# Optimization experiments

Measured on AMD Instinct MI355X. Metric: run time of the kernel, lower is better.

## Reference

```python
import jax, jax.numpy as jnp
from jax import lax
import numpy as np

EPS = 1e-5  # BatchNorm eps; eval-mode BN with running_mean=0, running_var=1


def _conv(x, w, b):
    return lax.conv_general_dilated(x, w, (1, 1), 'SAME', dimension_numbers=('NCHW', 'OIHW', 'NCHW')) + b[None, :, None, None]


def _cbr(x, w, b, g, a):
    # Conv -> BN(eval, mean=0, var=1) -> ReLU
    y = _conv(x, w, b)
    y = g[None, :, None, None] * (y * (1.0 / np.sqrt(1.0 + EPS))) + a[None, :, None, None]
    return jax.nn.relu(y)


def _pool(x):
    return lax.reduce_window(x, -jnp.inf, lax.max, (1, 1, 2, 2), (1, 1, 2, 2), 'VALID')


def _up2(x):
    B, C, H, W = x.shape
    Ho, Wo = 2 * H, 2 * W
    ys = jnp.arange(Ho) * ((H - 1) / (Ho - 1))
    xs = jnp.arange(Wo) * ((W - 1) / (Wo - 1))
    y0 = jnp.floor(ys).astype(jnp.int32); y1 = jnp.minimum(y0 + 1, H - 1)
    x0 = jnp.floor(xs).astype(jnp.int32); x1 = jnp.minimum(x0 + 1, W - 1)
    wy = (ys - y0).astype(x.dtype); wx = (xs - x0).astype(x.dtype)
    row = x[:, :, y0, :] * (1 - wy)[None, None, :, None] + x[:, :, y1, :] * wy[None, None, :, None]
    return row[:, :, :, x0] * (1 - wx) + row[:, :, :, x1] * wx


def _fcas(x, w, b):
    # FullyConnectedAtomicSpace: for each interior pixel (i,j) of x[0,1],
    # p = #(channel > v), n = #(channel == v), e = #(channel < v), out = (p*w0+b0 + n*w1+b1 + e*w2+b2)/3.
    # Vectorized via sort + searchsorted: O(N log N) instead of O(N^2).
    ch = x[0, 1]
    H, W = ch.shape
    flat = ch.ravel(); N = flat.size
    s = jnp.sort(flat)
    left = jnp.searchsorted(s, flat, side='left')
    right = jnp.searchsorted(s, flat, side='right')
    e = left.astype(x.dtype)            # count <
    n = (right - left).astype(x.dtype)  # count ==
    p = (N - right).astype(x.dtype)     # count >
    val = ((p * w[0] + b[0] + n * w[1] + b[1] + e * w[2] + b[2]) / 3.0).reshape(H, W)
    ii = jnp.arange(H); jj = jnp.arange(W)
    interior = ((ii >= 1) & (ii <= H - 2))[:, None] & ((jj >= 1) & (jj <= W - 2))[None, :]
    new_ch = jnp.where(interior, val, ch)
    # original converts to numpy and back -> detaches the whole tensor
    return lax.stop_gradient(x.at[0, 1].set(new_ch))


def _forward(x, w_inc, b_inc, g_inc, a_inc, w_d1, b_d1, g_d1, a_d1, w_d2, b_d2, g_d2, a_d2,
             w_d3, b_d3, g_d3, a_d3, w_u2, b_u2, g_u2, a_u2, w_u3, b_u3, g_u3, a_u3,
             w_u4, b_u4, g_u4, a_u4, w_out, b_out, fcas_w, fcas_b):
    x1 = _cbr(x, w_inc, b_inc, g_inc, a_inc)            # [B,8,512,512]
    x2 = _cbr(_pool(x1), w_d1, b_d1, g_d1, a_d1)        # [B,16,256,256]
    x3 = _cbr(_pool(x2), w_d2, b_d2, g_d2, a_d2)        # [B,32,128,128]
    x4 = _cbr(_pool(x3), w_d3, b_d3, g_d3, a_d3)        # [B,32,64,64]
    x4 = _fcas(x4, fcas_w, fcas_b)
    u = _cbr(jnp.concatenate([x3, _up2(x4)], axis=1), w_u2, b_u2, g_u2, a_u2)  # 64->16
    u = _cbr(jnp.concatenate([x2, _up2(u)], axis=1), w_u3, b_u3, g_u3, a_u3)   # 32->8
    u = _cbr(jnp.concatenate([x1, _up2(u)], axis=1), w_u4, b_u4, g_u4, a_u4)   # 16->4
    return jax.nn.sigmoid(_conv(u, w_out, b_out))       # [B,1,512,512]


def setup_inputs():
    key = jax.random.key(0)
    ks = jax.random.split(key, 24)
    d = {}
    d['x'] = jax.random.normal(ks[0], (8, 3, 512, 512), jnp.float32)
    specs = [('inc', 8, 3), ('d1', 16, 8), ('d2', 32, 16), ('d3', 32, 32), ('u2', 16, 64), ('u3', 8, 32), ('u4', 4, 16)]
    for idx, (nm, o, i) in enumerate(specs):
        k1, k2, k3, k4 = jax.random.split(ks[idx + 1], 4)
        d['w_' + nm] = jax.random.normal(k1, (o, i, 3, 3), jnp.float32) * 0.1
        d['b_' + nm] = jax.random.normal(k2, (o,), jnp.float32) * 0.1
        d['g_' + nm] = 1.0 + jax.random.normal(k3, (o,), jnp.float32) * 0.1
        d['a_' + nm] = jax.random.normal(k4, (o,), jnp.float32) * 0.1
    d['w_out'] = jax.random.normal(ks[20], (1, 4, 1, 1), jnp.float32) * 0.1
    d['b_out'] = jax.random.normal(ks[21], (1,), jnp.float32) * 0.1
    d['fcas_w'] = jnp.array([0.5, 0.5, 0.5], jnp.float32)
    d['fcas_b'] = jnp.array([0.5, 0.5, 0.5], jnp.float32)
    return d


def reference(x, w_inc, b_inc, g_inc, a_inc, w_d1, b_d1, g_d1, a_d1, w_d2, b_d2, g_d2, a_d2,
              w_d3, b_d3, g_d3, a_d3, w_u2, b_u2, g_u2, a_u2, w_u3, b_u3, g_u3, a_u3,
              w_u4, b_u4, g_u4, a_u4, w_out, b_out, fcas_w, fcas_b):
    return _forward(x, w_inc, b_inc, g_inc, a_inc, w_d1, b_d1, g_d1, a_d1, w_d2, b_d2, g_d2, a_d2,
                    w_d3, b_d3, g_d3, a_d3, w_u2, b_u2, g_u2, a_u2, w_u3, b_u3, g_u3, a_u3,
                    w_u4, b_u4, g_u4, a_u4, w_out, b_out, fcas_w, fcas_b)
```

## Files before the change

kernel.cpp:

```cpp
#include <hip/hip_runtime.h>
#include <hip/hip_bf16.h>

#define BN_RSQ 0.9999950000374997f

struct LayerP {
  const float* w; const float* b; const float* g; const float* a;
  float* wf; float* bf; int cout; int cin;
};
struct AllP { LayerP L[7]; float* zbuf; };

__global__ void prefold_kernel(AllP A) {
  LayerP p = A.L[blockIdx.y];
  int n = p.cout * p.cin * 9;
  int i = blockIdx.x * 256 + threadIdx.x;
  if (i < n) {
    int o = i / (p.cin * 9);
    p.wf[i] = p.w[i] * p.g[o] * BN_RSQ;
  }
  if (i < p.cout) p.bf[i] = p.b[i] * p.g[i] * BN_RSQ + p.a[i];
  if (blockIdx.y == 0 && blockIdx.x == 0 && i < 16) A.zbuf[i] = 0.f;
}

__device__ __forceinline__ void async_row_f32(const float* g, float* l) {
  __builtin_amdgcn_global_load_lds(
      (const __attribute__((address_space(1))) void*)g,
      (__attribute__((address_space(3))) void*)l, 4, 0, 0);
}

__global__ void up2_kernel(const float* __restrict__ in, float* __restrict__ out,
                           int Hi, int Wi) {
  const int Ho = 2 * Hi, Wo = 2 * Wi;
  const int ox = blockIdx.x * 16 + threadIdx.x;
  const int oy = blockIdx.y * 16 + threadIdx.y;
  const int bc = blockIdx.z;
  const float sy = (float)(Hi - 1) / (float)(Ho - 1);
  const float sx = (float)(Wi - 1) / (float)(Wo - 1);
  float fy = oy * sy, fx = ox * sx;
  int y0 = (int)floorf(fy); int y1 = min(y0 + 1, Hi - 1);
  int x0 = (int)floorf(fx); int x1 = min(x0 + 1, Wi - 1);
  float wy = fy - (float)y0, wx = fx - (float)x0;
  const float* p = in + (size_t)bc * Hi * Wi;
  float a00 = p[y0 * Wi + x0], a01 = p[y0 * Wi + x1];
  float a10 = p[y1 * Wi + x0], a11 = p[y1 * Wi + x1];
  float r0 = a00 * (1.f - wy) + a10 * wy;
  float r1 = a01 * (1.f - wy) + a11 * wy;
  out[((size_t)bc * Ho + oy) * Wo + ox] = r0 * (1.f - wx) + r1 * wx;
}

template <int CIN1, int CIN2, int COUTG, int OSPLIT, bool WRITE_POOL>
__launch_bounds__(256)
__global__ void conv3x3_direct(const float* __restrict__ in1,
                               const float* __restrict__ in2,
                               const float* __restrict__ wf,
                               const float* __restrict__ bf,
                               const float* __restrict__ zbuf,
                               float* __restrict__ out,
                               float* __restrict__ pout, int H, int W) {
  constexpr int CIN = CIN1 + CIN2;
  constexpr int COUT = COUTG * OSPLIT;
  __shared__ float wsm[COUTG * CIN * 12];

  const int tid = threadIdx.x;
  const int txp = (tid & 15) * 4;
  const int ty = tid >> 4;
  const int gx0 = blockIdx.x * 64;
  const int gy0 = blockIdx.y * 16;
  const int b = blockIdx.z & 7;
  const int og = blockIdx.z >> 3;
  const int obase = og * COUTG;
  const int lane = tid & 63;

  for (int idx = tid; idx < COUTG * CIN * 9; idx += 256) {
    int o = idx / (CIN * 9);
    int r = idx - o * (CIN * 9);
    int c = r / 9;
    int t = r - c * 9;
    wsm[(o * CIN + c) * 12 + t] = wf[((obase + o) * CIN + c) * 9 + t];
  }
  __syncthreads();

  const int ox = gx0 + txp;
  const int oy = gy0 + ty;
  const bool vM = (oy >= 1);
  const bool vP = (oy + 1 < H);
  const float selL = (ox >= 1) ? 1.f : 0.f;
  const float selR = (ox + 4 < W) ? 1.f : 0.f;
  const float* zp = zbuf + 4 - (size_t)ox;

  float acc[COUTG][4];
#pragma unroll
  for (int o = 0; o < COUTG; ++o)
#pragma unroll
    for (int i = 0; i < 4; ++i) acc[o][i] = 0.f;

  auto body = [&](const float* __restrict__ plane, int cabs) {
    const float* rC = plane + (size_t)oy * W;
    const float* rM = vM ? (rC - W) : zp;
    const float* rP = vP ? (rC + W) : zp;
    float rr[3][6];
#pragma unroll
    for (int dy = 0; dy < 3; ++dy) {
      const float* p = (dy == 0 ? rM : (dy == 1 ? rC : rP)) + ox;
      float4 v4 = *(const float4*)p;
      float lm = p[-1];
      float rp = p[4];
      rr[dy][0] = lm * selL;
      rr[dy][1] = v4.x; rr[dy][2] = v4.y; rr[dy][3] = v4.z; rr[dy][4] = v4.w;
      rr[dy][5] = rp * selR;
    }
#pragma unroll
    for (int o = 0; o < COUTG; ++o) {
      const float4* wp = (const float4*)&wsm[(o * CIN + cabs) * 12];
      float4 wa = wp[0];
      float4 wb = wp[1];
      float w8 = wsm[(o * CIN + cabs) * 12 + 8];
#pragma unroll
      for (int i = 0; i < 4; ++i) {
        float s = acc[o][i];
        s = fmaf(rr[0][i + 0], wa.x, s);
        s = fmaf(rr[0][i + 1], wa.y, s);
        s = fmaf(rr[0][i + 2], wa.z, s);
        s = fmaf(rr[1][i + 0], wa.w, s);
        s = fmaf(rr[1][i + 1], wb.x, s);
        s = fmaf(rr[1][i + 2], wb.y, s);
        s = fmaf(rr[2][i + 0], wb.z, s);
        s = fmaf(rr[2][i + 1], wb.w, s);
        s = fmaf(rr[2][i + 2], w8, s);
        acc[o][i] = s;
      }
    }
  };

#pragma unroll 1
  for (int c = 0; c < CIN1; ++c)
    body(in1 + (size_t)(b * CIN1 + c) * H * W, c);
  if (CIN2 > 0) {
#pragma unroll 1
    for (int c = 0; c < CIN2; ++c)
      body(in2 + (size_t)(b * CIN2 + c) * H * W, CIN1 + c);
  }

  const int H2 = H >> 1, W2 = W >> 1;
#pragma unroll
  for (int o = 0; o < COUTG; ++o) {
    float bo = bf[obase + o];
    float rv[4];
#pragma unroll
    for (int i = 0; i < 4; ++i) rv[i] = fmaxf(acc[o][i] + bo, 0.f);
    *(float4*)&out[((size_t)(b * COUT + obase + o) * H + oy) * W + ox] =
        *(float4*)rv;
    if (WRITE_POOL) {
      float m0 = fmaxf(rv[0], rv[1]);
      float m1 = fmaxf(rv[2], rv[3]);
      float q0 = fmaxf(m0, __shfl_down(m0, 16));
      float q1 = fmaxf(m1, __shfl_down(m1, 16));
      if (((lane >> 4) & 1) == 0) {
        float2 pw; pw.x = q0; pw.y = q1;
        *(float2*)&pout[((size_t)(b * COUT + obase + o) * H2 + (oy >> 1)) * W2 +
                        (ox >> 1)] = pw;
      }
    }
  }
}

__launch_bounds__(256)
__global__ void conv3x3_u4(const float* __restrict__ in1,
                           const float* __restrict__ in2,
                           const float* __restrict__ wf,
                           const float* __restrict__ bf,
                           const float* __restrict__ wout,
                           const float* __restrict__ bout,
                           const float* __restrict__ zbuf,
                           float* __restrict__ out) {
  constexpr int H = 512, W = 512, Hi = 256, Wi = 256;
  constexpr int CIN1 = 8, CIN2 = 8, CIN = 16, COUT = 4;
  __shared__ float utile[CIN2][18][68];
  __shared__ float wsm[COUT * CIN * 12];

  const int tid = threadIdx.x;
  const int lane = tid & 63;
  const int wv = tid >> 6;
  const int txp = (tid & 15) * 4;
  const int ty = tid >> 4;
  const int gx0 = blockIdx.x * 64;
  const int gy0 = blockIdx.y * 16;
  const int b = blockIdx.z;

  for (int idx = tid; idx < COUT * CIN * 9; idx += 256) {
    int o = idx / (CIN * 9);
    int r = idx - o * (CIN * 9);
    int c = r / 9;
    int t = r - c * 9;
    wsm[(o * CIN + c) * 12 + t] = wf[(o * CIN + c) * 9 + t];
  }

  const float sx = (float)(Wi - 1) / (float)(W - 1);
  const float sy = (float)(Hi - 1) / (float)(H - 1);
  const float* in2b = in2 + (size_t)b * CIN2 * Hi * Wi;

  {
    const int gox = gx0 + lane;
    const float fx = gox * sx;
    const int x0 = (int)fx;
    const int x1i = min(x0 + 1, Wi - 1);
    const float wx = fx - (float)x0;
    for (int t5 = wv; t5 < CIN2 * 18; t5 += 4) {
      const int c = t5 / 18;
      const int yy = t5 - c * 18;
      const int goy = gy0 + yy - 1;
      float v = 0.f;
      if (goy >= 0 && goy < H) {
        const float fy = goy * sy;
        const int y0 = (int)fy;
        const int y1 = min(y0 + 1, Hi - 1);
        const float wy = fy - (float)y0;
        const float* p0 = in2b + ((size_t)c * Hi + y0) * Wi;
        const float* p1 = in2b + ((size_t)c * Hi + y1) * Wi;
        float a00 = p0[x0], a01 = p0[x1i];
        float a10 = p1[x0], a11 = p1[x1i];
        float r0 = a00 * (1.f - wy) + a10 * wy;
        float r1 = a01 * (1.f - wy) + a11 * wy;
        v = r0 * (1.f - wx) + r1 * wx;
      }
      utile[c][yy][1 + lane] = v;
    }
  }
  for (int i = tid; i < 2 * CIN2 * 18; i += 256) {
    const int side = i & 1;
    const int row = i >> 1;
    const int c = row / 18;
    const int yy = row - c * 18;
    const int gox = side ? (gx0 + 64) : (gx0 - 1);
    const int goy = gy0 + yy - 1;
    float v = 0.f;
    if (goy >= 0 && goy < H && gox >= 0 && gox < W) {
      const float fy = goy * sy;
      const float fx = gox * sx;
      const int y0 = (int)fy;
      const int y1 = min(y0 + 1, Hi - 1);
      const int x0 = (int)fx;
      const int x1i = min(x0 + 1, Wi - 1);
      const float wy = fy - (float)y0;
      const float wx = fx - (float)x0;
      const float* p = in2b + (size_t)c * Hi * Wi;
      float a00 = p[y0 * Wi + x0], a01 = p[y0 * Wi + x1i];
      float a10 = p[y1 * Wi + x0], a11 = p[y1 * Wi + x1i];
      float r0 = a00 * (1.f - wy) + a10 * wy;
      float r1 = a01 * (1.f - wy) + a11 * wy;
      v = r0 * (1.f - wx) + r1 * wx;
    }
    utile[c][yy][side ? 65 : 0] = v;
  }
  __syncthreads();

  const int ox = gx0 + txp;
  const int oy = gy0 + ty;
  const bool vM = (oy >= 1);
  const bool vP = (oy + 1 < H);
  const float selL = (ox >= 1) ? 1.f : 0.f;
  const float selR = (ox + 4 < W) ? 1.f : 0.f;
  const float* zp = zbuf + 4 - (size_t)ox;

  float acc[COUT][4];
#pragma unroll
  for (int o = 0; o < COUT; ++o)
#pragma unroll
    for (int i = 0; i < 4; ++i) acc[o][i] = 0.f;

#pragma unroll 1
  for (int c = 0; c < CIN1; ++c) {
    const float* plane = in1 + (size_t)(b * CIN1 + c) * H * W;
    const float* rC = plane + (size_t)oy * W;
    const float* rM = vM ? (rC - W) : zp;
    const float* rP = vP ? (rC + W) : zp;
    float rr[3][6];
#pragma unroll
    for (int dy = 0; dy < 3; ++dy) {
      const float* p = (dy == 0 ? rM : (dy == 1 ? rC : rP)) + ox;
      float4 v4 = *(const float4*)p;
      float lm = p[-1];
      float rp = p[4];
      rr[dy][0] = lm * selL;
      rr[dy][1] = v4.x; rr[dy][2] = v4.y; rr[dy][3] = v4.z; rr[dy][4] = v4.w;
      rr[dy][5] = rp * selR;
    }
#pragma unroll
    for (int o = 0; o < COUT; ++o) {
      const float4* wp = (const float4*)&wsm[(o * CIN + c) * 12];
      float4 wa = wp[0];
      float4 wb = wp[1];
      float w8 = wsm[(o * CIN + c) * 12 + 8];
#pragma unroll
      for (int i = 0; i < 4; ++i) {
        float s = acc[o][i];
        s = fmaf(rr[0][i + 0], wa.x, s);
        s = fmaf(rr[0][i + 1], wa.y, s);
        s = fmaf(rr[0][i + 2], wa.z, s);
        s = fmaf(rr[1][i + 0], wa.w, s);
        s = fmaf(rr[1][i + 1], wb.x, s);
        s = fmaf(rr[1][i + 2], wb.y, s);
        s = fmaf(rr[2][i + 0], wb.z, s);
        s = fmaf(rr[2][i + 1], wb.w, s);
        s = fmaf(rr[2][i + 2], w8, s);
        acc[o][i] = s;
      }
    }
  }

#pragma unroll
  for (int c = 0; c < CIN2; ++c) {
    float rr[3][6];
#pragma unroll
    for (int dy = 0; dy < 3; ++dy) {
      const float* p = &utile[c][ty + dy][txp];
      float4 a4 = *(const float4*)p;
      float2 b2 = *(const float2*)(p + 4);
      rr[dy][0] = a4.x; rr[dy][1] = a4.y; rr[dy][2] = a4.z; rr[dy][3] = a4.w;
      rr[dy][4] = b2.x; rr[dy][5] = b2.y;
    }
    const int cabs = CIN1 + c;
#pragma unroll
    for (int o = 0; o < COUT; ++o) {
      const float4* wp = (const float4*)&wsm[(o * CIN + cabs) * 12];
      float4 wa = wp[0];
      float4 wb = wp[1];
      float w8 = wsm[(o * CIN + cabs) * 12 + 8];
#pragma unroll
      for (int i = 0; i < 4; ++i) {
        float s = acc[o][i];
        s = fmaf(rr[0][i + 0], wa.x, s);
        s = fmaf(rr[0][i + 1], wa.y, s);
        s = fmaf(rr[0][i + 2], wa.z, s);
        s = fmaf(rr[1][i + 0], wa.w, s);
        s = fmaf(rr[1][i + 1], wb.x, s);
        s = fmaf(rr[1][i + 2], wb.y, s);
        s = fmaf(rr[2][i + 0], wb.z, s);
        s = fmaf(rr[2][i + 1], wb.w, s);
        s = fmaf(rr[2][i + 2], w8, s);
        acc[o][i] = s;
      }
    }
  }

  float sv[4];
#pragma unroll
  for (int i = 0; i < 4; ++i) sv[i] = bout[0];
#pragma unroll
  for (int o = 0; o < COUT; ++o) {
    float bo = bf[o], wo = wout[o];
#pragma unroll
    for (int i = 0; i < 4; ++i) {
      float rr2 = fmaxf(acc[o][i] + bo, 0.f);
      sv[i] = fmaf(rr2, wo, sv[i]);
    }
  }
#pragma unroll
  for (int i = 0; i < 4; ++i) sv[i] = 1.f / (1.f + __expf(-sv[i]));
  *(float4*)&out[((size_t)b * H + oy) * W + ox] = *(float4*)sv;
}

template <int CIN1, int CIN2, int COUTG, int OSPLIT, bool UP_IN2, bool FUSE_OUT,
          bool WRITE_POOL>
__launch_bounds__(256)
__global__ void conv3x3_cbr(const float* __restrict__ in1,
                            const float* __restrict__ in2,
                            const float* __restrict__ wf,
                            const float* __restrict__ bf,
                            const float* __restrict__ wout,
                            const float* __restrict__ bout,
                            float* __restrict__ out,
                            float* __restrict__ pout, int H, int W) {
  constexpr int CIN = CIN1 + CIN2;
  constexpr int COUT = COUTG * OSPLIT;
  constexpr int PPT = 4;
  constexpr int CHUNK = (CIN < 4) ? CIN : 4;
  constexpr int XS = 68;
  constexpr int YT = 18;
  constexpr int ROWS = CHUNK * YT;

  __shared__ float tile[CHUNK][YT][XS];
  __shared__ float wsm[COUTG * CIN * 12];

  const int tid = threadIdx.x;
  const int txp = (tid & 15) * PPT;
  const int ty = tid >> 4;
  const int gx0 = blockIdx.x * 64;
  const int gy0 = blockIdx.y * 16;
  const int b = blockIdx.z & 7;
  const int og = blockIdx.z >> 3;
  const int obase = og * COUTG;

  const int lane = tid & 63;
  const int wv = tid >> 6;

  const int Hi = H >> 1, Wi = W >> 1;
  const float syf = UP_IN2 ? (float)(Hi - 1) / (float)(H - 1) : 0.f;

  int ux0 = 0, ux1 = 0;
  float uwx = 0.f;
  if (UP_IN2) {
    const float sx = (float)(Wi - 1) / (float)(W - 1);
    float fx = (gx0 + lane) * sx;
    ux0 = (int)fx;
    ux1 = min(ux0 + 1, Wi - 1);
    uwx = fx - (float)ux0;
  }

  for (int idx = tid; idx < COUTG * CIN * 9; idx += 256) {
    int o = idx / (CIN * 9);
    int r = idx - o * (CIN * 9);
    int c = r / 9;
    int t = r - c * 9;
    wsm[(o * CIN + c) * 12 + t] = wf[((obase + o) * CIN + c) * 9 + t];
  }

  float acc[COUTG][PPT];
#pragma unroll
  for (int o = 0; o < COUTG; ++o)
#pragma unroll
    for (int i = 0; i < PPT; ++i) acc[o][i] = 0.f;

  for (int cc = 0; cc < CIN; cc += CHUNK) {
    __syncthreads();
    if (wv < CHUNK) {
      const int c = wv;
      const int cg = cc + c;
      const bool dir1 = (CIN2 == 0 || cg < CIN1);
      if (dir1 || !UP_IN2) {
        const float* src;
        int cb;
        if (dir1) { src = in1; cb = b * CIN1 + cg; }
        else      { src = in2; cb = b * CIN2 + (cg - CIN1); }
        const float* base =
            src + (size_t)cb * H * W + (size_t)(gy0 - 1) * W + gx0 + lane;
#pragma unroll
        for (int yy = 0; yy < YT; ++yy) {
          const int iy = gy0 + yy - 1;
          if (iy >= 0 && iy < H) {
            async_row_f32(base + (size_t)yy * W, &tile[c][yy][1]);
          } else {
            tile[c][yy][1 + lane] = 0.f;
          }
        }
      } else {
        const int cb = b * CIN2 + (cg - CIN1);
#pragma unroll 1
        for (int yy = 0; yy < YT; ++yy) {
          const int iy = gy0 + yy - 1;
          float v = 0.f;
          if (iy >= 0 && iy < H) {
            float fy = iy * syf;
            int y0 = (int)fy;
            int y1 = min(y0 + 1, Hi - 1);
            float wy = fy - (float)y0;
            const float* r0p = in2 + (size_t)(cb * Hi + y0) * Wi;
            const float* r1p = in2 + (size_t)(cb * Hi + y1) * Wi;
            float a00 = r0p[ux0], a01 = r0p[ux1];
            float a10 = r1p[ux0], a11 = r1p[ux1];
            float r0 = a00 * (1.f - wy) + a10 * wy;
            float r1 = a01 * (1.f - wy) + a11 * wy;
            v = r0 * (1.f - uwx) + r1 * uwx;
          }
          tile[c][yy][1 + lane] = v;
        }
      }
    }
    for (int idx = tid; idx < 2 * ROWS; idx += 256) {
      const int row = idx >> 1;
      const int side = idx & 1;
      const int c = row / YT;
      const int yy = row - c * YT;
      const int iy = gy0 + yy - 1;
      const int ix = side ? (gx0 + 64) : (gx0 - 1);
      const int cg = cc + c;
      float v = 0.f;
      if (iy >= 0 && iy < H && ix >= 0 && ix < W) {
        if (CIN2 == 0 || cg < CIN1) {
          const int cb = b * CIN1 + cg;
          v = in1[(size_t)(cb * H + iy) * W + ix];
        } else if (UP_IN2) {
          const int cb = b * CIN2 + (cg - CIN1);
          const float sx = (float)(Wi - 1) / (float)(W - 1);
          float fy = iy * syf, fx = ix * sx;
          int y0 = (int)fy; int y1 = min(y0 + 1, Hi - 1);
          int x0 = (int)fx; int x1 = min(x0 + 1, Wi - 1);
          float wy = fy - (float)y0, wx = fx - (float)x0;
          const float* p = in2 + (size_t)cb * Hi * Wi;
          float a00 = p[y0 * Wi + x0], a01 = p[y0 * Wi + x1];
          float a10 = p[y1 * Wi + x0], a11 = p[y1 * Wi + x1];
          float r0 = a00 * (1.f - wy) + a10 * wy;
          float r1 = a01 * (1.f - wy) + a11 * wy;
          v = r0 * (1.f - wx) + r1 * wx;
        } else {
          const int cb = b * CIN2 + (cg - CIN1);
          v = in2[(size_t)(cb * H + iy) * W + ix];
        }
      }
      tile[c][yy][side ? 65 : 0] = v;
    }
    __syncthreads();
#pragma unroll
    for (int c = 0; c < CHUNK; ++c) {
      float rr[3][6];
#pragma unroll
      for (int dy = 0; dy < 3; ++dy) {
        const float* p = &tile[c][ty + dy][txp];
        float4 a4 = *(const float4*)p;
        float2 b2 = *(const float2*)(p + 4);
        rr[dy][0] = a4.x; rr[dy][1] = a4.y; rr[dy][2] = a4.z; rr[dy][3] = a4.w;
        rr[dy][4] = b2.x; rr[dy][5] = b2.y;
      }
      const int cabs = cc + c;
#pragma unroll
      for (int o = 0; o < COUTG; ++o) {
        const float4* wp = (const float4*)&wsm[(o * CIN + cabs) * 12];
        float4 wa = wp[0];
        float4 wb = wp[1];
        float w8 = wsm[(o * CIN + cabs) * 12 + 8];
#pragma unroll
        for (int i = 0; i < PPT; ++i) {
          float s = acc[o][i];
          s = fmaf(rr[0][i + 0], wa.x, s);
          s = fmaf(rr[0][i + 1], wa.y, s);
          s = fmaf(rr[0][i + 2], wa.z, s);
          s = fmaf(rr[1][i + 0], wa.w, s);
          s = fmaf(rr[1][i + 1], wb.x, s);
          s = fmaf(rr[1][i + 2], wb.y, s);
          s = fmaf(rr[2][i + 0], wb.z, s);
          s = fmaf(rr[2][i + 1], wb.w, s);
          s = fmaf(rr[2][i + 2], w8, s);
          acc[o][i] = s;
        }
      }
    }
  }

  const int oy = gy0 + ty;
  const int ox = gx0 + txp;
  if (FUSE_OUT) {
    float sv[PPT];
#pragma unroll
    for (int i = 0; i < PPT; ++i) sv[i] = bout[0];
#pragma unroll
    for (int o = 0; o < COUTG; ++o) {
      float bo = bf[obase + o], wo = wout[o];
#pragma unroll
      for (int i = 0; i < PPT; ++i) {
        float rr2 = fmaxf(acc[o][i] + bo, 0.f);
        sv[i] = fmaf(rr2, wo, sv[i]);
      }
    }
#pragma unroll
    for (int i = 0; i < PPT; ++i) sv[i] = 1.f / (1.f + __expf(-sv[i]));
    *(float4*)&out[((size_t)b * H + oy) * W + ox] = *(float4*)sv;
  } else {
    const int H2 = H >> 1, W2 = W >> 1;
#pragma unroll
    for (int o = 0; o < COUTG; ++o) {
      float bo = bf[obase + o];
      float rv[PPT];
#pragma unroll
      for (int i = 0; i < PPT; ++i) rv[i] = fmaxf(acc[o][i] + bo, 0.f);
      *(float4*)&out[((size_t)(b * COUT + obase + o) * H + oy) * W + ox] =
          *(float4*)rv;
      if (WRITE_POOL) {
        float m0 = fmaxf(rv[0], rv[1]);
        float m1 = fmaxf(rv[2], rv[3]);
        float q0 = fmaxf(m0, __shfl_down(m0, 16));
        float q1 = fmaxf(m1, __shfl_down(m1, 16));
        if (((lane >> 4) & 1) == 0) {
          float2 pw; pw.x = q0; pw.y = q1;
          *(float2*)&pout[((size_t)(b * COUT + obase + o) * H2 + (oy >> 1)) * W2 +
                          (ox >> 1)] = pw;
        }
      }
    }
  }
}

__global__ void fcas_partial(const float* __restrict__ ch,
                             int* __restrict__ pcnt, int* __restrict__ ncnt) {
  __shared__ float sv[256];
  const int e = blockIdx.x * 256 + threadIdx.x;
  const int s = blockIdx.y;
  sv[threadIdx.x] = ch[s * 256 + threadIdx.x];
  __syncthreads();
  const float v = ch[e];
  int p = 0, n = 0;
#pragma unroll 4
  for (int k = 0; k < 256; ++k) {
    float u = sv[k];
    p += (u > v);
    n += (u == v);
  }
  pcnt[s * 4096 + e] = p;
  ncnt[s * 4096 + e] = n;
}

__global__ void fcas_final(float* __restrict__ ch,
                           const int* __restrict__ pcnt,
                           const int* __restrict__ ncnt,
                           const float* __restrict__ w,
                           const float* __restrict__ bb) {
  const int e = blockIdx.x * 256 + threadIdx.x;
  int p = 0, n = 0;
#pragma unroll
  for (int s = 0; s < 16; ++s) {
    p += pcnt[s * 4096 + e];
    n += ncnt[s * 4096 + e];
  }
  const int el = 4096 - p - n;
  float val = ((float)p * w[0] + bb[0] + (float)n * w[1] + bb[1] +
               (float)el * w[2] + bb[2]) / 3.0f;
  int i = e >> 6, j = e & 63;
  bool interior = (i >= 1) && (i <= 62) && (j >= 1) && (j <= 62);
  if (interior) ch[e] = val;
}

extern "C" void kernel_launch(void* const* d_in, const int* in_sizes, int n_in,
                              void* d_out, int out_size, void* d_ws, size_t ws_size,
                              hipStream_t stream) {
  const float* x      = (const float*)d_in[0];
  const float* w_inc  = (const float*)d_in[1];
  const float* b_inc  = (const float*)d_in[2];
  const float* g_inc  = (const float*)d_in[3];
  const float* a_inc  = (const float*)d_in[4];
  const float* w_d1   = (const float*)d_in[5];
  const float* b_d1   = (const float*)d_in[6];
  const float* g_d1   = (const float*)d_in[7];
  const float* a_d1   = (const float*)d_in[8];
  const float* w_d2   = (const float*)d_in[9];
  const float* b_d2   = (const float*)d_in[10];
  const float* g_d2   = (const float*)d_in[11];
  const float* a_d2   = (const float*)d_in[12];
  const float* w_d3   = (const float*)d_in[13];
  const float* b_d3   = (const float*)d_in[14];
  const float* g_d3   = (const float*)d_in[15];
  const float* a_d3   = (const float*)d_in[16];
  const float* w_u2   = (const float*)d_in[17];
  const float* b_u2   = (const float*)d_in[18];
  const float* g_u2   = (const float*)d_in[19];
  const float* a_u2   = (const float*)d_in[20];
  const float* w_u3   = (const float*)d_in[21];
  const float* b_u3   = (const float*)d_in[22];
  const float* g_u3   = (const float*)d_in[23];
  const float* a_u3   = (const float*)d_in[24];
  const float* w_u4   = (const float*)d_in[25];
  const float* b_u4   = (const float*)d_in[26];
  const float* g_u4   = (const float*)d_in[27];
  const float* a_u4   = (const float*)d_in[28];
  const float* w_out  = (const float*)d_in[29];
  const float* b_out  = (const float*)d_in[30];
  const float* fcas_w = (const float*)d_in[31];
  const float* fcas_b = (const float*)d_in[32];

  float* ws = (float*)d_ws;
  float* zbuf   = ws;
  float* wf_inc = ws + 16;
  float* wf_d1  = wf_inc + 216;
  float* wf_d2  = wf_d1 + 1152;
  float* wf_d3  = wf_d2 + 4608;
  float* wf_u2  = wf_d3 + 9216;
  float* wf_u3  = wf_u2 + 9216;
  float* wf_u4  = wf_u3 + 2304;
  float* bf_inc = wf_u4 + 576;
  float* bf_d1  = bf_inc + 8;
  float* bf_d2  = bf_d1 + 16;
  float* bf_d3  = bf_d2 + 32;
  float* bf_u2  = bf_d3 + 32;
  float* bf_u3  = bf_u2 + 16;
  float* bf_u4  = bf_u3 + 8;
  int*   pcnt   = (int*)(ws + 27424);
  int*   ncnt   = pcnt + 65536;
  float* x1  = (float*)(ncnt + 65536);
  float* p1  = x1 + 16777216;
  float* x2  = p1 + 4194304;
  float* p2  = x2 + 8388608;
  float* x3  = p2 + 2097152;
  float* p3  = x3 + 4194304;
  float* x4  = p3 + 1048576;
  float* upa = x4 + 1048576;
  float* uo2 = upa + 4194304;
  float* uo3 = uo2 + 2097152;
  float* upb = x3;
  float* outp = (float*)d_out;

  AllP A;
  A.L[0] = {w_inc, b_inc, g_inc, a_inc, wf_inc, bf_inc, 8, 3};
  A.L[1] = {w_d1, b_d1, g_d1, a_d1, wf_d1, bf_d1, 16, 8};
  A.L[2] = {w_d2, b_d2, g_d2, a_d2, wf_d2, bf_d2, 32, 16};
  A.L[3] = {w_d3, b_d3, g_d3, a_d3, wf_d3, bf_d3, 32, 32};
  A.L[4] = {w_u2, b_u2, g_u2, a_u2, wf_u2, bf_u2, 16, 64};
  A.L[5] = {w_u3, b_u3, g_u3, a_u3, wf_u3, bf_u3, 8, 32};
  A.L[6] = {w_u4, b_u4, g_u4, a_u4, wf_u4, bf_u4, 4, 16};
  A.zbuf = zbuf;
  prefold_kernel<<<dim3(36, 7), dim3(256), 0, stream>>>(A);

  dim3 blk(256);
  dim3 blk2(16, 16);

  conv3x3_cbr<3, 0, 8, 1, false, false, true><<<dim3(8, 32, 8), blk, 0, stream>>>(
      x, nullptr, wf_inc, bf_inc, nullptr, nullptr, x1, p1, 512, 512);
  conv3x3_direct<8, 0, 4, 4, true><<<dim3(4, 16, 32), blk, 0, stream>>>(
      p1, nullptr, wf_d1, bf_d1, zbuf, x2, p2, 256, 256);
  conv3x3_direct<16, 0, 4, 8, true><<<dim3(2, 8, 64), blk, 0, stream>>>(
      p2, nullptr, wf_d2, bf_d2, zbuf, x3, p3, 128, 128);
  conv3x3_direct<32, 0, 2, 16, false><<<dim3(1, 4, 128), blk, 0, stream>>>(
      p3, nullptr, wf_d3, bf_d3, zbuf, x4, nullptr, 64, 64);
  fcas_partial<<<dim3(16, 16), blk, 0, stream>>>(x4 + 4096, pcnt, ncnt);
  fcas_final<<<dim3(16), blk, 0, stream>>>(x4 + 4096, pcnt, ncnt, fcas_w, fcas_b);
  up2_kernel<<<dim3(8, 8, 256), blk2, 0, stream>>>(x4, upa, 64, 64);
  conv3x3_direct<32, 32, 2, 8, false><<<dim3(2, 8, 64), blk, 0, stream>>>(
      x3, upa, wf_u2, bf_u2, zbuf, uo2, nullptr, 128, 128);
  up2_kernel<<<dim3(16, 16, 128), blk2, 0, stream>>>(uo2, upb, 128, 128);
  conv3x3_direct<16, 16, 2, 4, false><<<dim3(4, 16, 32), blk, 0, stream>>>(
      x2, upb, wf_u3, bf_u3, zbuf, uo3, nullptr, 256, 256);
  conv3x3_u4<<<dim3(8, 32, 8), blk, 0, stream>>>(
      x1, uo3, wf_u4, bf_u4, w_out, b_out, zbuf, outp);
}
```

Before: 484.5 us.

## Stage upsampled skip channels in two halves to shrink LDS tile

The final u4 conv kernel now builds the bilinear-upsampled tile for 4 channels at a time instead of all 8, halving that LDS buffer, and computes on each half in turn with extra barriers in between. The staging loop is also restructured so each wave computes the row interpolation once and reuses it across the 4 channels, and the halo columns are assigned to fixed threads. The smaller shared-memory footprint is meant to allow more resident blocks per CU and to cut redundant index math. In exchange there are two more __syncthreads and a second staging phase that the direct in1 loads do not overlap.

Result: slower. 537.6 us (+11.0%).

```diff
diff --git a/kernel.cpp b/kernel.cpp
--- a/kernel.cpp
+++ b/kernel.cpp
@@ -174,7 +174,8 @@
                            float* __restrict__ out) {
   constexpr int H = 512, W = 512, Hi = 256, Wi = 256;
   constexpr int CIN1 = 8, CIN2 = 8, CIN = 16, COUT = 4;
-  __shared__ float utile[CIN2][18][68];
+  constexpr int CH = 4;
+  __shared__ float utile[CH][18][68];
   __shared__ float wsm[COUT * CIN * 12];
 
   const int tid = threadIdx.x;
@@ -198,60 +199,61 @@
   const float sy = (float)(Hi - 1) / (float)(H - 1);
   const float* in2b = in2 + (size_t)b * CIN2 * Hi * Wi;
 
-  {
-    const int gox = gx0 + lane;
-    const float fx = gox * sx;
-    const int x0 = (int)fx;
-    const int x1i = min(x0 + 1, Wi - 1);
-    const float wx = fx - (float)x0;
-    for (int t5 = wv; t5 < CIN2 * 18; t5 += 4) {
-      const int c = t5 / 18;
-      const int yy = t5 - c * 18;
+  const float fxL = (float)(gx0 + lane) * sx;
+  const int x0L = (int)fxL;
+  const int x1L = min(x0L + 1, Wi - 1);
+  const float wxL = fxL - (float)x0L;
+
+  const int hc = tid >> 6;
+  const int hside = (tid >> 5) & 1;
+  const int hyy = tid & 31;
+  const int hgox = hside ? (gx0 + 64) : (gx0 - 1);
+  const float hfx = (float)hgox * sx;
+  const int hx0 = (int)hfx;
+  const int hx1 = min(hx0 + 1, Wi - 1);
+  const float hwx = hfx - (float)hx0;
+
+  auto stage = [&](int cbase) {
+    for (int yy = wv; yy < 18; yy += 4) {
       const int goy = gy0 + yy - 1;
-      float v = 0.f;
       if (goy >= 0 && goy < H) {
-        const float fy = goy * sy;
+        const float fy = (float)goy * sy;
         const int y0 = (int)fy;
         const int y1 = min(y0 + 1, Hi - 1);
         const float wy = fy - (float)y0;
-        const float* p0 = in2b + ((size_t)c * Hi + y0) * Wi;
-        const float* p1 = in2b + ((size_t)c * Hi + y1) * Wi;
-        float a00 = p0[x0], a01 = p0[x1i];
-        float a10 = p1[x0], a11 = p1[x1i];
+        const int r0o = y0 * Wi, r1o = y1 * Wi;
+#pragma unroll
+        for (int c = 0; c < CH; ++c) {
+          const float* pc = in2b + (size_t)(cbase + c) * (Hi * Wi);
+          float a00 = pc[r0o + x0L], a01 = pc[r0o + x1L];
+          float a10 = pc[r1o + x0L], a11 = pc[r1o + x1L];
+          float r0 = a00 * (1.f - wy) + a10 * wy;
+          float r1 = a01 * (1.f - wy) + a11 * wy;
+          utile[c][yy][1 + lane] = r0 * (1.f - wxL) + r1 * wxL;
+        }
+      } else {
+#pragma unroll
+        for (int c = 0; c < CH; ++c) utile[c][yy][1 + lane] = 0.f;
+      }
+    }
+    if (hyy < 18) {
+      const int goy = gy0 + hyy - 1;
+      float v = 0.f;
+      if (goy >= 0 && goy < H && hgox >= 0 && hgox < W) {
+        const float fy = (float)goy * sy;
+        const int y0 = (int)fy;
+        const int y1 = min(y0 + 1, Hi - 1);
+        const float wy = fy - (float)y0;
+        const float* pc = in2b + (size_t)(cbase + hc) * (Hi * Wi);
+        float a00 = pc[y0 * Wi + hx0], a01 = pc[y0 * Wi + hx1];
+        float a10 = pc[y1 * Wi + hx0], a11 = pc[y1 * Wi + hx1];
         float r0 = a00 * (1.f - wy) + a10 * wy;
         float r1 = a01 * (1.f - wy) + a11 * wy;
-        v = r0 * (1.f - wx) + r1 * wx;
-      }
-      utile[c][yy][1 + lane] = v;
-    }
-  }
-  for (int i = tid; i < 2 * CIN2 * 18; i += 256) {
-    const int side = i & 1;
-    const int row = i >> 1;
-    const int c = row / 18;
-    const int yy = row - c * 18;
-    const int gox = side ? (gx0 + 64) : (gx0 - 1);
-    const int goy = gy0 + yy - 1;
-    float v = 0.f;
-    if (goy >= 0 && goy < H && gox >= 0 && gox < W) {
-      const float fy = goy * sy;
-      const float fx = gox * sx;
-      const int y0 = (int)fy;
-      const int y1 = min(y0 + 1, Hi - 1);
-      const int x0 = (int)fx;
-      const int x1i = min(x0 + 1, Wi - 1);
-      const float wy = fy - (float)y0;
-      const float wx = fx - (float)x0;
-      const float* p = in2b + (size_t)c * Hi * Wi;
-      float a00 = p[y0 * Wi + x0], a01 = p[y0 * Wi + x1i];
-      float a10 = p[y1 * Wi + x0], a11 = p[y1 * Wi + x1i];
-      float r0 = a00 * (1.f - wy) + a10 * wy;
-      float r1 = a01 * (1.f - wy) + a11 * wy;
-      v = r0 * (1.f - wx) + r1 * wx;
-    }
-    utile[c][yy][side ? 65 : 0] = v;
-  }
-  __syncthreads();
+        v = r0 * (1.f - hwx) + r1 * hwx;
+      }
+      utile[hc][hyy][hside ? 65 : 0] = v;
+    }
+  };
 
   const int ox = gx0 + txp;
   const int oy = gy0 + ty;
@@ -266,6 +268,46 @@
   for (int o = 0; o < COUT; ++o)
 #pragma unroll
     for (int i = 0; i < 4; ++i) acc[o][i] = 0.f;
+
+  auto compute_phase = [&](int cbase) {
+#pragma unroll
+    for (int c = 0; c < CH; ++c) {
+      float rr[3][6];
+#pragma unroll
+      for (int dy = 0; dy < 3; ++dy) {
+        const float* p = &utile[c][ty + dy][txp];
+        float4 a4 = *(const float4*)p;
+        float2 b2 = *(const float2*)(p + 4);
+        rr[dy][0] = a4.x; rr[dy][1] = a4.y; rr[dy][2] = a4.z; rr[dy][3] = a4.w;
+        rr[dy][4] = b2.x; rr[dy][5] = b2.y;
+      }
+      const int cabs = CIN1 + cbase + c;
+#pragma unroll
+      for (int o = 0; o < COUT; ++o) {
+        const float4* wp = (const float4*)&wsm[(o * CIN + cabs) * 12];
+        float4 wa = wp[0];
+        float4 wb = wp[1];
+        float w8 = wsm[(o * CIN + cabs) * 12 + 8];
+#pragma unroll
+        for (int i = 0; i < 4; ++i) {
+          float s = acc[o][i];
+          s = fmaf(rr[0][i + 0], wa.x, s);
+          s = fmaf(rr[0][i + 1], wa.y, s);
+          s = fmaf(rr[0][i + 2], wa.z, s);
+          s = fmaf(rr[1][i + 0], wa.w, s);
+          s = fmaf(rr[1][i + 1], wb.x, s);
+          s = fmaf(rr[1][i + 2], wb.y, s);
+          s = fmaf(rr[2][i + 0], wb.z, s);
+          s = fmaf(rr[2][i + 1], wb.w, s);
+          s = fmaf(rr[2][i + 2], w8, s);
+          acc[o][i] = s;
+        }
+      }
+    }
+  };
+
+  stage(0);
+  __syncthreads();
 
 #pragma unroll 1
   for (int c = 0; c < CIN1; ++c) {
@@ -307,40 +349,11 @@
     }
   }
 
-#pragma unroll
-  for (int c = 0; c < CIN2; ++c) {
-    float rr[3][6];
-#pragma unroll
-    for (int dy = 0; dy < 3; ++dy) {
-      const float* p = &utile[c][ty + dy][txp];
-      float4 a4 = *(const float4*)p;
-      float2 b2 = *(const float2*)(p + 4);
-      rr[dy][0] = a4.x; rr[dy][1] = a4.y; rr[dy][2] = a4.z; rr[dy][3] = a4.w;
-      rr[dy][4] = b2.x; rr[dy][5] = b2.y;
-    }
-    const int cabs = CIN1 + c;
-#pragma unroll
-    for (int o = 0; o < COUT; ++o) {
-      const float4* wp = (const float4*)&wsm[(o * CIN + cabs) * 12];
-      float4 wa = wp[0];
-      float4 wb = wp[1];
-      float w8 = wsm[(o * CIN + cabs) * 12 + 8];
-#pragma unroll
-      for (int i = 0; i < 4; ++i) {
-        float s = acc[o][i];
-        s = fmaf(rr[0][i + 0], wa.x, s);
-        s = fmaf(rr[0][i + 1], wa.y, s);
-        s = fmaf(rr[0][i + 2], wa.z, s);
-        s = fmaf(rr[1][i + 0], wa.w, s);
-        s = fmaf(rr[1][i + 1], wb.x, s);
-        s = fmaf(rr[1][i + 2], wb.y, s);
-        s = fmaf(rr[2][i + 0], wb.z, s);
-        s = fmaf(rr[2][i + 1], wb.w, s);
-        s = fmaf(rr[2][i + 2], w8, s);
-        acc[o][i] = s;
-      }
-    }
-  }
+  compute_phase(0);
+  __syncthreads();
+  stage(CH);
+  __syncthreads();
+  compute_phase(CH);
 
   float sv[4];
 #pragma unroll
```
